# Performance work log

Measured on AMD Instinct MI355X. Metric: run time of the kernel, lower is better.

Reference implementation:

```python
import jax, jax.numpy as jnp
import numpy as np

N, D, C, K, M = 32768, 512, 64, 16, 128
DEPTH = 4            # log2(K): decision-tree depth per codebook
NODES = K - 1        # 15 internal tree nodes per codebook


def _build_selection_matrix():
    # Node i of the binary tree lives at level log2(i+1) and thresholds the
    # level-l selected dimension of its codebook.
    S = np.zeros((C * NODES, C * DEPTH), dtype=np.float32)
    base = np.zeros((NODES, DEPTH), dtype=np.float32)
    for i in range(NODES):
        base[i, int(np.log2(i + 1))] = 1.0
    for c in range(C):
        S[c * NODES:(c + 1) * NODES, c * DEPTH:(c + 1) * DEPTH] = base
    return S


def _build_bit_matrix():
    # Leaf k scores +1/-1 on each of its DEPTH ancestor nodes; the true leaf
    # attains the maximal score DEPTH.
    base = np.zeros((K, NODES), dtype=np.float32)
    for k in range(K):
        for l in range(DEPTH):
            node = (1 << l) - 1 + (k >> (DEPTH - l))   # ancestor at level l
            bit = (k >> (DEPTH - 1 - l)) & 1            # right(1)/left(0)
            base[k, node] = 1.0 if bit else -1.0
    B = np.zeros((C * K, C * NODES), dtype=np.float32)
    for c in range(C):
        B[c * K:(c + 1) * K, c * NODES:(c + 1) * NODES] = base
    return B


def setup_inputs() -> dict:
    key = jax.random.key(0)
    k1, k2, k3, k4 = jax.random.split(key, 4)
    I = jax.random.normal(k1, (N, D), jnp.float32)
    T = jax.random.normal(k2, (C * NODES,), jnp.float32) * 0.1   # thresholds
    L = jax.random.normal(k3, (M, C, K), jnp.float32)            # LUT
    dims = jnp.sort(jax.random.randint(k4, (C * DEPTH,), 0, D))  # selected cols
    S = jnp.asarray(_build_selection_matrix())
    B = jnp.asarray(_build_bit_matrix())
    temp = jnp.ones((1,), jnp.float32)
    return {"I": I, "T": T, "L": L, "S": S, "B": B, "dims": dims, "temp": temp}


def reference(I, T, L, S, B, dims, temp):
    t = temp[0]
    x_sel = I[:, dims]                                  # (N, C*DEPTH) gather
    h = x_sel @ S.T - T                                 # (N, C*NODES)
    tanh_h = jnp.tanh(h / t)
    # straight-through sign: forward sign(h), backward d(tanh(h/t))
    sign_ste = jnp.sign(h) - jax.lax.stop_gradient(tanh_h) + tanh_h
    b = sign_ste @ B.T                                  # (N, C*K) leaf scores
    soft = jax.nn.softmax(b.reshape(-1, C, K) / t, axis=2)
    hard = jax.nn.one_hot(jnp.argmax(soft, axis=2), K, dtype=soft.dtype)
    # straight-through one-hot encoding E: forward hard, backward soft
    E = hard - jax.lax.stop_gradient(soft) + soft       # (N, C, K)
    return jnp.einsum("nck,mck->nm", E, L)              # LUT gather-sum readout
```

## Files before the change

kernel.cpp:

```cpp
#include <hip/hip_runtime.h>

#define N_TOTAL 32768
#define D_DIM   512
#define C_DIM   64
#define K_DIM   16
#define M_DIM   128
#define NODES_  15
#define ROWS    16

typedef unsigned short u16;
typedef unsigned int   u32;

__device__ __forceinline__ u32 f2bf_bits(float f) {
    u32 u = __float_as_uint(f);
    return (u + 0x7FFFu + ((u >> 16) & 1u)) >> 16;
}
__device__ __forceinline__ float bf_lo(u32 u) { return __uint_as_float(u << 16); }
__device__ __forceinline__ float bf_hi(u32 u) { return __uint_as_float(u & 0xFFFF0000u); }

__global__ __launch_bounds__(256) void build_lut_kernel(
    const float* __restrict__ L, u16* __restrict__ LUT)
{
    int idx = blockIdx.x * 256 + threadIdx.x;
    int q  = idx & 15;
    int kk = (idx >> 4) & 255;
    int p  = idx >> 12;
    int c0 = (2 * p) * 16 + (kk & 15);
    int c1 = (2 * p + 1) * 16 + (kk >> 4);
    u32 w[4];
    #pragma unroll
    for (int h = 0; h < 4; ++h) {
        int m0 = q * 8 + 2 * h;
        float a0 = L[m0 * 1024 + c0]       + L[m0 * 1024 + c1];
        float a1 = L[(m0 + 1) * 1024 + c0] + L[(m0 + 1) * 1024 + c1];
        w[h] = f2bf_bits(a0) | (f2bf_bits(a1) << 16);
    }
    *(uint4*)(LUT + (size_t)((p << 8) | kk) * M_DIM + q * 8) =
        make_uint4(w[0], w[1], w[2], w[3]);
}

__global__ __launch_bounds__(256) void fused_kernel(
    const float* __restrict__ I,
    const float* __restrict__ T,
    const int* __restrict__ dims,
    const u16* __restrict__ LUT,
    float* __restrict__ out)
{
    __shared__ float sT[C_DIM * NODES_];
    __shared__ int   sDims[C_DIM * 4];
    __shared__ int   sCode[ROWS * 65];

    const int tid = threadIdx.x;
    const int n0  = blockIdx.x * ROWS;

    sDims[tid] = dims[tid];
    for (int j = tid; j < C_DIM * NODES_; j += 256) sT[j] = T[j];
    __syncthreads();

    for (int t = tid; t < ROWS * C_DIM; t += 256) {
        int row = t >> 6;
        int c   = t & 63;
        const float* v = I + (size_t)(n0 + row) * D_DIM;
        int node = 0, k = 0;
        #pragma unroll
        for (int l = 0; l < 4; ++l) {
            float h = v[sDims[(c << 2) + l]] - sT[c * NODES_ + node];
            int bit = (h > 0.0f) ? 1 : 0;
            k = (k << 1) | bit;
            node = (node << 1) + 1 + bit;
        }
        sCode[row * 65 + c] = k;
    }
    __syncthreads();

    const int r = tid >> 4;
    const int q = tid & 15;
    const int* codeRow = sCode + r * 65;

    float4 acc0 = make_float4(0.f, 0.f, 0.f, 0.f);
    float4 acc1 = make_float4(0.f, 0.f, 0.f, 0.f);

    #pragma unroll
    for (int p = 0; p < 32; ++p) {
        u32 kk = (u32)codeRow[2 * p] | ((u32)codeRow[2 * p + 1] << 4);
        const uint4 v = *(const uint4*)(LUT + (size_t)(((p << 8) | kk) << 7) + (q << 3));
        acc0.x += bf_lo(v.x); acc0.y += bf_hi(v.x);
        acc0.z += bf_lo(v.y); acc0.w += bf_hi(v.y);
        acc1.x += bf_lo(v.z); acc1.y += bf_hi(v.z);
        acc1.z += bf_lo(v.w); acc1.w += bf_hi(v.w);
    }

    float4* o = (float4*)(out + (size_t)(n0 + r) * M_DIM + (q << 3));
    o[0] = acc0;
    o[1] = acc1;
}

extern "C" void kernel_launch(void* const* d_in, const int* in_sizes, int n_in,
                              void* d_out, int out_size, void* d_ws, size_t ws_size,
                              hipStream_t stream) {
    const float* I    = (const float*)d_in[0];
    const float* T    = (const float*)d_in[1];
    const float* L    = (const float*)d_in[2];
    const int*   dims = (const int*)d_in[5];

    u16* LUT = (u16*)d_ws;

    hipLaunchKernelGGL(build_lut_kernel, dim3(512), dim3(256), 0, stream, L, LUT);
    hipLaunchKernelGGL(fused_kernel, dim3(N_TOTAL / ROWS), dim3(256), 0, stream,
                       I, T, dims, LUT, (float*)d_out);
}
```

Before: 125.0 us.

## Keep tree codes in registers per wave and share them via readlane

Each wave now handles four rows. Each lane computes the tree codes for one codebook across those four rows and packs them into one register. The codes are then broadcast with readlane instead of passing through shared memory, which removes the sCode array and a block barrier. The dims are loaded once per lane as an int4 and the input gathers are issued before the threshold staging, so more loads are in flight. The cost is scalar readlane traffic inside the LUT loop, plus 32-bit LUT offset arithmetic.

```diff
diff --git a/kernel.cpp b/kernel.cpp
--- a/kernel.cpp
+++ b/kernel.cpp
@@ -47,50 +47,62 @@
     float* __restrict__ out)
 {
     __shared__ float sT[C_DIM * NODES_];
-    __shared__ int   sDims[C_DIM * 4];
-    __shared__ int   sCode[ROWS * 65];
 
-    const int tid = threadIdx.x;
-    const int n0  = blockIdx.x * ROWS;
+    const int tid  = threadIdx.x;
+    const int lane = tid & 63;
+    const int wv   = tid >> 6;
+    const int rowBase = blockIdx.x * ROWS + wv * 4;
 
-    sDims[tid] = dims[tid];
+    const int4 dml = ((const int4*)dims)[lane];
+
+    float vv[4][4];
+    #pragma unroll
+    for (int rr = 0; rr < 4; ++rr) {
+        const float* v = I + (size_t)(rowBase + rr) * D_DIM;
+        vv[rr][0] = v[dml.x];
+        vv[rr][1] = v[dml.y];
+        vv[rr][2] = v[dml.z];
+        vv[rr][3] = v[dml.w];
+    }
+
     for (int j = tid; j < C_DIM * NODES_; j += 256) sT[j] = T[j];
     __syncthreads();
 
-    for (int t = tid; t < ROWS * C_DIM; t += 256) {
-        int row = t >> 6;
-        int c   = t & 63;
-        const float* v = I + (size_t)(n0 + row) * D_DIM;
+    const float* tc = sT + lane * NODES_;
+    u32 cp = 0;
+    #pragma unroll
+    for (int rr = 0; rr < 4; ++rr) {
         int node = 0, k = 0;
         #pragma unroll
         for (int l = 0; l < 4; ++l) {
-            float h = v[sDims[(c << 2) + l]] - sT[c * NODES_ + node];
+            float h = vv[rr][l] - tc[node];
             int bit = (h > 0.0f) ? 1 : 0;
             k = (k << 1) | bit;
             node = (node << 1) + 1 + bit;
         }
-        sCode[row * 65 + c] = k;
+        cp |= (u32)k << (4 * rr);
     }
-    __syncthreads();
 
-    const int r = tid >> 4;
-    const int q = tid & 15;
-    const int* codeRow = sCode + r * 65;
+    const int r   = lane >> 4;
+    const int q   = lane & 15;
+    const int rsh = r * 4;
 
     float4 acc0 = make_float4(0.f, 0.f, 0.f, 0.f);
     float4 acc1 = make_float4(0.f, 0.f, 0.f, 0.f);
 
     #pragma unroll
     for (int p = 0; p < 32; ++p) {
-        u32 kk = (u32)codeRow[2 * p] | ((u32)codeRow[2 * p + 1] << 4);
-        const uint4 v = *(const uint4*)(LUT + (size_t)(((p << 8) | kk) << 7) + (q << 3));
+        u32 ca = (u32)__builtin_amdgcn_readlane((int)cp, 2 * p);
+        u32 cb = (u32)__builtin_amdgcn_readlane((int)cp, 2 * p + 1);
+        u32 kk = ((ca >> rsh) & 15u) | (((cb >> rsh) & 15u) << 4);
+        const uint4 v = *(const uint4*)(LUT + (((p << 8) | kk) << 7) + (q << 3));
         acc0.x += bf_lo(v.x); acc0.y += bf_hi(v.x);
         acc0.z += bf_lo(v.y); acc0.w += bf_hi(v.y);
         acc1.x += bf_lo(v.z); acc1.y += bf_hi(v.z);
         acc1.z += bf_lo(v.w); acc1.w += bf_hi(v.w);
     }
 
-    float4* o = (float4*)(out + (size_t)(n0 + r) * M_DIM + (q << 3));
+    float4* o = (float4*)(out + (size_t)(rowBase + r) * M_DIM + (q << 3));
     o[0] = acc0;
     o[1] = acc1;
 }
```

Measured after the change: 126.4 us. No clear change (+1.1%).
